# Performance work log

Measured on AMD Instinct MI355X. Metric: run time of the kernel, lower is better.

## Reference

```python
import jax, jax.numpy as jnp
import numpy as np

B, T, D = 2, 2048, 1024
NH, NKV, HD = 16, 4, 64
BASE, TSL, QGI = 10000.0, 1024, 1.5
EPS = 1.1920929e-07  # torch.finfo(float32).eps used by F.rms_norm default


def _rope_cos_sin(seq_len, rd):
    # Rotary.forward with self.rd == head_dim (Attn sets rd=0 -> full rotation)
    if seq_len > TSL:  # NTK-style base rescale branch
        nb = BASE * (seq_len / TSL) ** (rd / (rd - 2))
    else:
        nb = BASE
    inv = 1.0 / nb ** (jnp.arange(0, rd, 2, dtype=jnp.float32) / rd)
    fr = jnp.arange(seq_len, dtype=jnp.float32)[:, None] * inv[None, :]
    return jnp.cos(fr)[None, :, None, :], jnp.sin(fr)[None, :, None, :]


def _apply_rope(x, cos, sin):
    h = x.shape[-1] // 2
    x1, x2 = x[..., :h], x[..., h:]
    return jnp.concatenate([x1 * cos + x2 * sin, -x1 * sin + x2 * cos], axis=-1)


def _rms_norm(x):
    return x * jax.lax.rsqrt(jnp.mean(x * x, axis=-1, keepdims=True) + EPS)


def setup_inputs() -> dict:
    key = jax.random.key(0)
    ks = jax.random.split(key, 8)
    s = jnp.float32(0.02)
    return {
        "x": jax.random.normal(ks[0], (B, T, D), jnp.float32),
        "qw": jax.random.normal(ks[1], (NH * HD, D), jnp.float32) * s,
        "kw": jax.random.normal(ks[2], (NKV * HD, D), jnp.float32) * s,
        "vw": jax.random.normal(ks[3], (NKV * HD, D), jnp.float32) * s,
        "ow": jax.random.normal(ks[4], (D, D), jnp.float32) * s,
        "ve": jax.random.normal(ks[5], (B, T, NKV * HD), jnp.float32) * s,
        "v0": jax.random.normal(ks[6], (B, T, NKV, HD), jnp.float32) * s,
        "q_gain": jnp.full((NH,), QGI, jnp.float32),
        "vr_lambda": jnp.array([0.5, 0.5], jnp.float32),
        "gate_w": jnp.zeros((NH, D), jnp.float32),      # nn.init.zeros_
        "gate_b": jnp.full((NH,), 4.0, jnp.float32),    # nn.init.constant_(4.0)
    }


def reference(x, qw, kw, vw, ow, ve, v0, q_gain, vr_lambda, gate_w, gate_b):
    # projections
    q = (x @ qw.T).reshape(B, T, NH, HD)
    k = (x @ kw.T).reshape(B, T, NKV, HD)
    v = (x @ vw.T + ve).reshape(B, T, NKV, HD)
    raw_v = v  # returned when vr=True
    v = vr_lambda[0] * v0 + vr_lambda[1] * v  # value residual
    # qk rms-norm + rope (full head dim since self.rd == 0) + per-head q gain
    q = _rms_norm(q)
    k = _rms_norm(k)
    cos, sin = _rope_cos_sin(T, HD)
    q = _apply_rope(q, cos, sin)
    k = _apply_rope(k, cos, sin)
    q = q * q_gain[None, None, :, None]
    # causal GQA attention (nh query heads share nkv kv heads)
    G = NH // NKV
    qg = q.reshape(B, T, NKV, G, HD)
    scale = 1.0 / np.sqrt(HD).astype(np.float32)
    scores = jnp.einsum('bqhgd,bkhd->bhgqk', qg, k) * scale  # [B,NKV,G,T,T]
    causal = jnp.tril(jnp.ones((T, T), bool))
    scores = jnp.where(causal[None, None, None], scores, jnp.finfo(scores.dtype).min)
    p = jax.nn.softmax(scores, axis=-1)
    y = jnp.einsum('bhgqk,bkhd->bqhgd', p, v).reshape(B, T, NH, HD)
    # gated attention output
    gate = jax.nn.sigmoid(x @ gate_w.T + gate_b)  # [B,T,NH]
    y = y * gate[..., None]
    out = y.reshape(B, T, D) @ ow.T
    return out, raw_v
```

## Files before the change

### kernel.cpp

```cpp
#include <hip/hip_runtime.h>
#include <math.h>

#define BB 2
#define TT 2048
#define DD 1024
#define NH 16
#define NKV 4
#define HD 64
#define EPSF 1.1920929e-07f
#define LOG2_NB 14.319970444065578
#define SCALE_LOG2E 0.18033688011112042f
#define FIXMAX 17.5f

typedef __attribute__((ext_vector_type(8))) short bf16x8;
typedef __attribute__((ext_vector_type(4))) float f32x4;

__device__ inline short f2bf(float f) {
    unsigned u = __builtin_bit_cast(unsigned, f);
    unsigned r = (u + 0x7fffu + ((u >> 16) & 1u)) >> 16;
    return (short)r;
}
__device__ inline unsigned cvt_pk_bf16(float a, float b) {
    unsigned r;
    asm("v_cvt_pk_bf16_f32 %0, %1, %2" : "=v"(r) : "v"(a), "v"(b));
    return r;
}

__global__ __launch_bounds__(256) void conv_all(
    const float* __restrict__ x, const float* __restrict__ qw,
    const float* __restrict__ kw, const float* __restrict__ vw,
    const float* __restrict__ ow,
    short* __restrict__ x16, short* __restrict__ wb16, short* __restrict__ ow16)
{
    int i = blockIdx.x * 256 + threadIdx.x;
    const float* src; short* dst; int j;
    if (i < 1048576)      { src = x;  dst = x16;            j = i; }
    else if (i < 1310720) { src = qw; dst = wb16;           j = i - 1048576; }
    else if (i < 1376256) { src = kw; dst = wb16 + 1048576; j = i - 1310720; }
    else if (i < 1441792) { src = vw; dst = wb16 + 1310720; j = i - 1376256; }
    else                  { src = ow; dst = ow16;           j = i - 1441792; }
    float4 v = ((const float4*)src)[j];
    short4 o;
    o.x = f2bf(v.x); o.y = f2bf(v.y); o.z = f2bf(v.z); o.w = f2bf(v.w);
    ((short4*)dst)[j] = o;
}

__global__ __launch_bounds__(256, 4) void gemm_mfma(
    const short* __restrict__ A, const short* __restrict__ Bmat,
    float* __restrict__ C, int ldc, int klen)
{
    __shared__ short As[2][128*32];
    __shared__ short Bs[2][128*32];
    int tid = threadIdx.x;
    int w = tid >> 6, lane = tid & 63;
    int quad = lane >> 4, lc = lane & 15;
    int wy = w >> 1, wx = w & 1;
    int m0 = blockIdx.y * 128, n0 = blockIdx.x * 128;
    int kbeg = blockIdx.z * klen, kend = kbeg + klen;
    float* Cz = C + (size_t)blockIdx.z * 4096 * ldc;

    f32x4 acc[4][4];
    #pragma unroll
    for (int i = 0; i < 4; i++)
        #pragma unroll
        for (int j = 0; j < 4; j++) acc[i][j] = (f32x4){0.f,0.f,0.f,0.f};

    #define GSTAGE(buf, k0)                                                             \
    {                                                                                   \
        _Pragma("unroll")                                                               \
        for (int i = 0; i < 2; i++) {                                                   \
            int off = w*2048 + i*1024;                   \
            int g = (off >> 4) + lane;                               \
            int row = g >> 2, c = g & 3;                                                \
            int cg = c ^ (row & 3);                                    \
            const short* ga = A + (size_t)(m0 + row)*1024 + (k0) + cg*8;                \
            __builtin_amdgcn_global_load_lds(                                           \
                (const __attribute__((address_space(1))) void*)ga,                      \
                (__attribute__((address_space(3))) void*)((char*)&As[buf][0] + off), 16, 0, 0); \
            const short* gb = Bmat + (size_t)(n0 + row)*1024 + (k0) + cg*8;             \
            __builtin_amdgcn_global_load_lds(                                           \
                (const __attribute__((address_space(1))) void*)gb,                      \
                (__attribute__((address_space(3))) void*)((char*)&Bs[buf][0] + off), 16, 0, 0); \
        }                                                                               \
    }

    GSTAGE(0, kbeg);
    __syncthreads();

    for (int k0 = kbeg; k0 < kend; k0 += 32) {
        int cur = ((k0 - kbeg) >> 5) & 1;

        bf16x8 af[4], bfr[4];
        #pragma unroll
        for (int tm = 0; tm < 4; tm++) {
            int row = wy*64 + tm*16 + lc;
            af[tm] = *(const bf16x8*)(&As[cur][0] + row*32 + ((quad*8) ^ ((row&3)*8)));
        }
        #pragma unroll
        for (int tn = 0; tn < 4; tn++) {
            int row = wx*64 + tn*16 + lc;
            bfr[tn] = *(const bf16x8*)(&Bs[cur][0] + row*32 + ((quad*8) ^ ((row&3)*8)));
        }
        if (k0 + 32 < kend) GSTAGE(cur ^ 1, k0 + 32);
        #pragma unroll
        for (int tm = 0; tm < 4; tm++)
            #pragma unroll
            for (int tn = 0; tn < 4; tn++)
                acc[tm][tn] = __builtin_amdgcn_mfma_f32_16x16x32_bf16(af[tm], bfr[tn], acc[tm][tn], 0, 0, 0);
        __syncthreads();
    }

    #pragma unroll
    for (int tm = 0; tm < 4; tm++)
        #pragma unroll
        for (int r = 0; r < 4; r++) {
            int m = m0 + wy*64 + tm*16 + quad*4 + r;
            #pragma unroll
            for (int tn = 0; tn < 4; tn++) {
                int n = n0 + wx*64 + tn*16 + lc;
                Cz[(size_t)m*ldc + n] = acc[tm][tn][r];
            }
        }
}

__global__ __launch_bounds__(256) void qkv_epilogue(
    const float* __restrict__ qp0, const float* __restrict__ qp1,
    const float* __restrict__ ve, const float* __restrict__ v0,
    const float* __restrict__ q_gain, const float* __restrict__ vr_lambda,
    short* __restrict__ qbh, short* __restrict__ kbh, short* __restrict__ vb,
    float* __restrict__ rawv)
{
    int wave = blockIdx.x * 4 + (threadIdx.x >> 6);
    int lane = threadIdx.x & 63;
    int row = wave / 24;
    int hh  = wave % 24;
    int b = row >> 11;
    int t = row & (TT - 1);

    if (hh < 20) {
        int col = (hh < 16) ? (hh*64 + lane) : (1024 + (hh-16)*64 + lane);
        size_t idx = (size_t)row*1536 + col;
        float val = qp0[idx] + qp1[idx];
        float ss = val * val;
        #pragma unroll
        for (int off = 32; off; off >>= 1) ss += __shfl_xor(ss, off);
        val *= rsqrtf(ss * (1.0f/64.0f) + EPSF);
        float partner = __shfl(val, lane ^ 32);
        int idxr = lane & 31;
        float inv = (float)exp2((double)idxr * (-LOG2_NB / 32.0));
        float fr = (float)t * inv;
        float sn, cs;
        sincosf(fr, &sn, &cs);
        float outv = (lane < 32) ? (val*cs + partner*sn) : (val*cs - partner*sn);
        if (hh < 16) {
            outv *= q_gain[hh] * SCALE_LOG2E;
            qbh[(((size_t)(b*16 + hh))*2048 + t)*64 + lane] = f2bf(outv);
        } else {
            kbh[(((size_t)(b*4 + (hh-16)))*2048 + t)*64 + lane] = f2bf(outv);
        }
    } else {
        int vh = hh - 20;
        size_t off = ((size_t)row*4 + vh)*64 + lane;
        size_t idx = (size_t)row*1536 + 1280 + vh*64 + lane;
        float vraw = qp0[idx] + qp1[idx] + ve[off];
        rawv[off] = vraw;
        float vmix = vr_lambda[0]*v0[off] + vr_lambda[1]*vraw;
        vb[off] = f2bf(vmix);
    }
}

__global__ __launch_bounds__(256) void transpose_v(
    const short* __restrict__ vb, short* __restrict__ vtb)
{
    __shared__ short tile[64][72];
    int bk = blockIdx.x;
    int tt = blockIdx.y;
    int b = bk >> 2, kvh = bk & 3;
    int tid = threadIdx.x;
    int t4 = tid >> 4;
    int d4 = (tid & 15) * 4;
    #pragma unroll
    for (int i = 0; i < 4; i++) {
        int t = t4 + i*16;
        const short* src = vb + (((size_t)(b*2048 + tt*64 + t)*4 + kvh)*64 + d4);
        *(short4*)&tile[t][d4] = *(const short4*)src;
    }
    __syncthreads();
    #pragma unroll
    for (int i = 0; i < 4; i++) {
        int d = t4 + i*16;
        int t0 = d4;
        short4 o;
        o.x = tile[t0+0][d]; o.y = tile[t0+1][d];
        o.z = tile[t0+2][d]; o.w = tile[t0+3][d];
        *(short4*)&vtb[((size_t)(bk*64 + d))*2048 + tt*64 + t0] = o;
    }
}

__global__ __launch_bounds__(256) void gate_kernel(
    const float* __restrict__ x, const float* __restrict__ gw,
    const float* __restrict__ gb, float* __restrict__ gate)
{
    __shared__ float xs[1024];
    int row = blockIdx.x;
    int tid = threadIdx.x;
    *(float4*)&xs[tid*4] = *(const float4*)&x[(size_t)row*1024 + tid*4];
    __syncthreads();
    int wave = tid >> 6, lane = tid & 63;
    for (int h = wave; h < 16; h += 4) {
        const float* w = gw + (size_t)h * 1024;
        float s = 0.f;
        #pragma unroll
        for (int i = 0; i < 16; i++) s += xs[lane + 64*i] * w[lane + 64*i];
        #pragma unroll
        for (int off = 32; off; off >>= 1) s += __shfl_xor(s, off);
        if (lane == 0) gate[(size_t)row*16 + h] = 1.0f / (1.0f + __expf(-(s + gb[h])));
    }
}

__global__ __launch_bounds__(256, 4) void flash_mfma(
    const short* __restrict__ qbh, const short* __restrict__ kbh,
    const short* __restrict__ vtb, const float* __restrict__ gate,
    short* __restrict__ y16)
{
    __shared__ short Ks[2][64*64];
    __shared__ short Vt[2][64*64];
    __shared__ short Ps[4][16*64];

    int bh = blockIdx.x;
    int b = bh >> 4, h = bh & 15, kvh = h >> 2;
    int qt = 31 - blockIdx.y;
    int tid = threadIdx.x;
    int w = tid >> 6, lane = tid & 63;
    int quad = lane >> 4, lc = lane & 15;

    const short* qbase = qbh + (((size_t)bh)*2048 + qt*64 + w*16 + lc)*64;
    bf16x8 qf0 = *(const bf16x8*)(qbase + quad*8);
    bf16x8 qf1 = *(const bf16x8*)(qbase + 32 + quad*8);

    f32x4 o[4];
    #pragma unroll
    for (int i = 0; i < 4; i++) o[i] = (f32x4){0.f,0.f,0.f,0.f};
    f32x4 l4 = (f32x4){0.f,0.f,0.f,0.f};
    const bf16x8 ones = {(short)0x3F80,(short)0x3F80,(short)0x3F80,(short)0x3F80,
                         (short)0x3F80,(short)0x3F80,(short)0x3F80,(short)0x3F80};

    const size_t kbase = ((size_t)(b*4 + kvh))*2048*64;
    const size_t vbase = ((size_t)(b*4 + kvh))*64*2048;

    #define STAGE(buf, kt)                                                              \
    {                                                                                   \
        _Pragma("unroll")                                                               \
        for (int i = 0; i < 2; i++) {                                                   \
            int off = w*2048 + i*1024;                                                  \
            int g = (off >> 4) + lane;                                                  \
            int row = g >> 3, c = g & 7;                                                \
            int cg = c ^ (row & 7);                                                     \
            const short* gk = kbh + kbase + (size_t)((kt)*64 + row)*64 + cg*8;          \
            __builtin_amdgcn_global_load_lds(                                           \
                (const __attribute__((address_space(1))) void*)gk,                      \
                (__attribute__((address_space(3))) void*)((char*)Ks[buf] + off), 16, 0, 0); \
            const short* gv = vtb + vbase + (size_t)row*2048 + (kt)*64 + cg*8;          \
            __builtin_amdgcn_global_load_lds(                                           \
                (const __attribute__((address_space(1))) void*)gv,                      \
                (__attribute__((address_space(3))) void*)((char*)Vt[buf] + off), 16, 0, 0); \
        }                                                                               \
    }

    STAGE(0, 0);
    __syncthreads();

    short* ps = Ps[w];

    for (int kt = 0; kt <= qt; kt++) {
        int cur = kt & 1;
        bool diag = (kt == qt);

        bf16x8 kf0[4], kf1[4], vf0[4], vf1[4];
        #pragma unroll
        for (int kn = 0; kn < 4; kn++) {
            int row = kn*16 + lc;
            int sw = (row & 7) * 8;
            const short* kr = Ks[cur] + row*64;
            kf0[kn] = *(const bf16x8*)(kr + ((quad*8) ^ sw));
            kf1[kn] = *(const bf16x8*)(kr + ((quad*8 + 32) ^ sw));
            const short* vr = Vt[cur] + row*64;
            vf0[kn] = *(const bf16x8*)(vr + ((quad*8) ^ sw));
            vf1[kn] = *(const bf16x8*)(vr + ((quad*8 + 32) ^ sw));
        }
        if (kt < qt) STAGE(cur ^ 1, kt + 1);

        f32x4 s4[4];
        #pragma unroll
        for (int kn = 0; kn < 4; kn++) {
            f32x4 acc = (f32x4){0.f,0.f,0.f,0.f};
            acc = __builtin_amdgcn_mfma_f32_16x16x32_bf16(kf0[kn], qf0, acc, 0, 0, 0);
            acc = __builtin_amdgcn_mfma_f32_16x16x32_bf16(kf1[kn], qf1, acc, 0, 0, 0);
            s4[kn] = acc;
        }

        #pragma unroll
        for (int kn = 0; kn < 4; kn++) {
            float p0 = __builtin_amdgcn_exp2f(s4[kn][0] - FIXMAX);
            float p1 = __builtin_amdgcn_exp2f(s4[kn][1] - FIXMAX);
            float p2 = __builtin_amdgcn_exp2f(s4[kn][2] - FIXMAX);
            float p3 = __builtin_amdgcn_exp2f(s4[kn][3] - FIXMAX);
            if (diag) {
                int keyb = kn*16 + quad*4, qv = w*16 + lc;
                if (keyb + 0 > qv) p0 = 0.f;
                if (keyb + 1 > qv) p1 = 0.f;
                if (keyb + 2 > qv) p2 = 0.f;
                if (keyb + 3 > qv) p3 = 0.f;
            }
            int c = kn*4 + quad;
            int cs = c ^ ((lc & 7) << 1);
            int2 pk;
            pk.x = (int)cvt_pk_bf16(p0, p1);
            pk.y = (int)cvt_pk_bf16(p2, p3);
            *(int2*)(ps + lc*64 + cs*4) = pk;
        }
        __asm__ volatile("s_waitcnt lgkmcnt(0)" ::: "memory");
        int u0 = (0*4 + quad) ^ (lc & 7);
        int u1 = (1*4 + quad) ^ (lc & 7);
        bf16x8 pf0 = *(const bf16x8*)(ps + lc*64 + u0*8);
        bf16x8 pf1 = *(const bf16x8*)(ps + lc*64 + u1*8);

        #pragma unroll
        for (int dn = 0; dn < 4; dn++) {
            o[dn] = __builtin_amdgcn_mfma_f32_16x16x32_bf16(pf0, vf0[dn], o[dn], 0, 0, 0);
            o[dn] = __builtin_amdgcn_mfma_f32_16x16x32_bf16(pf1, vf1[dn], o[dn], 0, 0, 0);
        }
        l4 = __builtin_amdgcn_mfma_f32_16x16x32_bf16(pf0, ones, l4, 0, 0, 0);
        l4 = __builtin_amdgcn_mfma_f32_16x16x32_bf16(pf1, ones, l4, 0, 0, 0);
        __syncthreads();
    }

    #pragma unroll
    for (int r = 0; r < 4; r++) {
        int row = b*2048 + qt*64 + w*16 + quad*4 + r;
        float g = gate[(size_t)row*16 + h] / l4[r];
        #pragma unroll
        for (int dn = 0; dn < 4; dn++)
            y16[(size_t)row*1024 + h*64 + dn*16 + lc] = f2bf(o[dn][r] * g);
    }
}

extern "C" void kernel_launch(void* const* d_in, const int* in_sizes, int n_in,
                              void* d_out, int out_size, void* d_ws, size_t ws_size,
                              hipStream_t stream) {
    (void)in_sizes; (void)n_in; (void)out_size; (void)ws_size;
    const float* x  = (const float*)d_in[0];
    const float* qw = (const float*)d_in[1];
    const float* kw = (const float*)d_in[2];
    const float* vw = (const float*)d_in[3];
    const float* ow = (const float*)d_in[4];
    const float* ve = (const float*)d_in[5];
    const float* v0 = (const float*)d_in[6];
    const float* qg = (const float*)d_in[7];
    const float* vl = (const float*)d_in[8];
    const float* gw = (const float*)d_in[9];
    const float* gb = (const float*)d_in[10];

    float* out  = (float*)d_out;
    float* rawv = out + (size_t)BB*TT*DD;

    float* ws   = (float*)d_ws;
    float* qkvp = ws;
    float* p    = ws + 2*6291456;
    short* x16  = (short*)p;        p += 2097152;
    short* wb16 = (short*)p;        p += 786432;
    short* ow16 = (short*)p;        p += 524288;
    short* qbh  = (short*)p;        p += 2097152;
    short* kbh  = (short*)p;        p += 524288;
    short* vtb  = (short*)p;        p += 524288;
    short* vb   = (short*)p;        p += 524288;
    float* gt   = p;
    short* y16  = (short*)qkvp;

    conv_all<<<6656, 256, 0, stream>>>(x, qw, kw, vw, ow, x16, wb16, ow16);
    gemm_mfma<<<dim3(12, 32, 2), 256, 0, stream>>>(x16, wb16, qkvp, 1536, 512);
    qkv_epilogue<<<24576, 256, 0, stream>>>(qkvp, qkvp + 6291456, ve, v0, qg, vl,
                                            qbh, kbh, vb, rawv);
    transpose_v<<<dim3(8, 32), 256, 0, stream>>>(vb, vtb);
    gate_kernel<<<4096, 256, 0, stream>>>(x, gw, gb, gt);
    flash_mfma<<<dim3(32, 32), 256, 0, stream>>>(qbh, kbh, vtb, gt, y16);
    gemm_mfma<<<dim3(8, 32, 1), 256, 0, stream>>>(y16, ow16, out, 1024, 1024);
}
```

Baseline: 211.1 us.

## Fuse QKV epilogue into QKV GEMM and drop split-K partial buffers

The separate QKV epilogue kernel is replaced by an epilogue inside the QKV GEMM. It applies RMS-norm, RoPE, q gain and the value residual directly from the accumulators, using shuffles across the 16-lane column group. Split-K over two z-slices is removed, so the fp32 partial sums are no longer written and re-read, though the grid shrinks from 768 to 384 blocks and launch bounds drop to 3. The gate kernel now reads the bf16 copy of x instead of fp32, which loses some precision in the gate logits.

New measurement: 199.8 us. 1.06x faster.

```diff
diff --git a/kernel.cpp b/kernel.cpp
--- a/kernel.cpp
+++ b/kernel.cpp
@@ -19,6 +19,10 @@
     unsigned u = __builtin_bit_cast(unsigned, f);
     unsigned r = (u + 0x7fffu + ((u >> 16) & 1u)) >> 16;
     return (short)r;
+}
+__device__ inline float bf2f(short s) {
+    unsigned u = ((unsigned)(unsigned short)s) << 16;
+    return __builtin_bit_cast(float, u);
 }
 __device__ inline unsigned cvt_pk_bf16(float a, float b) {
     unsigned r;
@@ -45,9 +49,56 @@
     ((short4*)dst)[j] = o;
 }
 
-__global__ __launch_bounds__(256, 4) void gemm_mfma(
+#define GSTAGE(buf, k0, Abase, Bbase)                                                   \
+{                                                                                       \
+    _Pragma("unroll")                                                                   \
+    for (int i_ = 0; i_ < 2; i_++) {                                                    \
+        int off = w*2048 + i_*1024;                      \
+        int g = (off >> 4) + lane;                                   \
+        int row = g >> 2, c = g & 3;                                                    \
+        int cg = c ^ (row & 3);                                        \
+        const short* ga = (Abase) + (size_t)(m0 + row)*1024 + (k0) + cg*8;              \
+        __builtin_amdgcn_global_load_lds(                                               \
+            (const __attribute__((address_space(1))) void*)ga,                          \
+            (__attribute__((address_space(3))) void*)((char*)&As[buf][0] + off), 16, 0, 0); \
+        const short* gb = (Bbase) + (size_t)(n0 + row)*1024 + (k0) + cg*8;              \
+        __builtin_amdgcn_global_load_lds(                                               \
+            (const __attribute__((address_space(1))) void*)gb,                          \
+            (__attribute__((address_space(3))) void*)((char*)&Bs[buf][0] + off), 16, 0, 0); \
+    }                                                                                   \
+}
+
+#define GEMM_MAIN_LOOP(kbeg, kend, Abase, Bbase)                                        \
+    GSTAGE(0, (kbeg), (Abase), (Bbase));                                                \
+    __syncthreads();                                                                    \
+    for (int k0 = (kbeg); k0 < (kend); k0 += 32) {                                      \
+        int cur = ((k0 - (kbeg)) >> 5) & 1;                                             \
+        bf16x8 af[4], bfr[4];                                                           \
+        _Pragma("unroll")                                                               \
+        for (int tm = 0; tm < 4; tm++) {                                                \
+            int row = wy*64 + tm*16 + lc;                                               \
+            af[tm] = *(const bf16x8*)(&As[cur][0] + row*32 + ((quad*8) ^ ((row&3)*8))); \
+        }                                                                               \
+        _Pragma("unroll")                                                               \
+        for (int tn = 0; tn < 4; tn++) {                                                \
+            int row = wx*64 + tn*16 + lc;                                               \
+            bfr[tn] = *(const bf16x8*)(&Bs[cur][0] + row*32 + ((quad*8) ^ ((row&3)*8))); \
+        }                                                                               \
+        if (k0 + 32 < (kend)) GSTAGE(cur ^ 1, k0 + 32, (Abase), (Bbase));               \
+        _Pragma("unroll")                                                               \
+        for (int tm = 0; tm < 4; tm++)                                                  \
+            _Pragma("unroll")                                                           \
+            for (int tn = 0; tn < 4; tn++)                                              \
+                acc[tm][tn] = __builtin_amdgcn_mfma_f32_16x16x32_bf16(af[tm], bfr[tn], acc[tm][tn], 0, 0, 0); \
+        __syncthreads();                                                                \
+    }
+
+__global__ __launch_bounds__(256, 3) void gemm_qkv_fused(
     const short* __restrict__ A, const short* __restrict__ Bmat,
-    float* __restrict__ C, int ldc, int klen)
+    const float* __restrict__ ve, const float* __restrict__ v0,
+    const float* __restrict__ q_gain, const float* __restrict__ vr_lambda,
+    short* __restrict__ qbh, short* __restrict__ kbh, short* __restrict__ vb,
+    float* __restrict__ rawv)
 {
     __shared__ short As[2][128*32];
     __shared__ short Bs[2][128*32];
@@ -56,8 +107,6 @@
     int quad = lane >> 4, lc = lane & 15;
     int wy = w >> 1, wx = w & 1;
     int m0 = blockIdx.y * 128, n0 = blockIdx.x * 128;
-    int kbeg = blockIdx.z * klen, kend = kbeg + klen;
-    float* Cz = C + (size_t)blockIdx.z * 4096 * ldc;
 
     f32x4 acc[4][4];
     #pragma unroll
@@ -65,50 +114,85 @@
         #pragma unroll
         for (int j = 0; j < 4; j++) acc[i][j] = (f32x4){0.f,0.f,0.f,0.f};
 
-    #define GSTAGE(buf, k0)                                                             \
-    {                                                                                   \
-        _Pragma("unroll")                                                               \
-        for (int i = 0; i < 2; i++) {                                                   \
-            int off = w*2048 + i*1024;                   \
-            int g = (off >> 4) + lane;                               \
-            int row = g >> 2, c = g & 3;                                                \
-            int cg = c ^ (row & 3);                                    \
-            const short* ga = A + (size_t)(m0 + row)*1024 + (k0) + cg*8;                \
-            __builtin_amdgcn_global_load_lds(                                           \
-                (const __attribute__((address_space(1))) void*)ga,                      \
-                (__attribute__((address_space(3))) void*)((char*)&As[buf][0] + off), 16, 0, 0); \
-            const short* gb = Bmat + (size_t)(n0 + row)*1024 + (k0) + cg*8;             \
-            __builtin_amdgcn_global_load_lds(                                           \
-                (const __attribute__((address_space(1))) void*)gb,                      \
-                (__attribute__((address_space(3))) void*)((char*)&Bs[buf][0] + off), 16, 0, 0); \
-        }                                                                               \
-    }
-
-    GSTAGE(0, kbeg);
-    __syncthreads();
-
-    for (int k0 = kbeg; k0 < kend; k0 += 32) {
-        int cur = ((k0 - kbeg) >> 5) & 1;
-
-        bf16x8 af[4], bfr[4];
+    GEMM_MAIN_LOOP(0, 1024, A, Bmat);
+
+    int hc = n0 + wx*64;
+    if (hc < 1280) {
+        bool isq = (hc < 1024);
+        int h = isq ? (hc >> 6) : ((hc - 1024) >> 6);
+        float gsc = isq ? (q_gain[h] * SCALE_LOG2E) : 1.0f;
+        short* dst = isq ? qbh : kbh;
+        int nhh = isq ? 16 : 4;
+        float inv0 = (float)exp2((double)lc * (-LOG2_NB / 32.0));
+        float inv1 = (float)exp2((double)(lc + 16) * (-LOG2_NB / 32.0));
         #pragma unroll
         for (int tm = 0; tm < 4; tm++) {
-            int row = wy*64 + tm*16 + lc;
-            af[tm] = *(const bf16x8*)(&As[cur][0] + row*32 + ((quad*8) ^ ((row&3)*8)));
-        }
-        #pragma unroll
-        for (int tn = 0; tn < 4; tn++) {
-            int row = wx*64 + tn*16 + lc;
-            bfr[tn] = *(const bf16x8*)(&Bs[cur][0] + row*32 + ((quad*8) ^ ((row&3)*8)));
-        }
-        if (k0 + 32 < kend) GSTAGE(cur ^ 1, k0 + 32);
-        #pragma unroll
-        for (int tm = 0; tm < 4; tm++)
             #pragma unroll
-            for (int tn = 0; tn < 4; tn++)
-                acc[tm][tn] = __builtin_amdgcn_mfma_f32_16x16x32_bf16(af[tm], bfr[tn], acc[tm][tn], 0, 0, 0);
-        __syncthreads();
-    }
+            for (int r = 0; r < 4; r++) {
+                int m = m0 + wy*64 + tm*16 + quad*4 + r;
+                int b = m >> 11, t = m & (TT - 1);
+                float a0 = acc[tm][0][r], a1 = acc[tm][1][r];
+                float a2 = acc[tm][2][r], a3 = acc[tm][3][r];
+                float ss = a0*a0 + a1*a1 + a2*a2 + a3*a3;
+                ss += __shfl_xor(ss, 1);
+                ss += __shfl_xor(ss, 2);
+                ss += __shfl_xor(ss, 4);
+                ss += __shfl_xor(ss, 8);
+                float rn = rsqrtf(ss * (1.0f/64.0f) + EPSF);
+                a0 *= rn; a1 *= rn; a2 *= rn; a3 *= rn;
+                float sn0, cs0, sn1, cs1;
+                sincosf((float)t * inv0, &sn0, &cs0);
+                sincosf((float)t * inv1, &sn1, &cs1);
+                float o0 = a0*cs0 + a2*sn0;
+                float o1 = a1*cs1 + a3*sn1;
+                float o2 = a2*cs0 - a0*sn0;
+                float o3 = a3*cs1 - a1*sn1;
+                size_t base = (((size_t)(b*nhh + h))*2048 + t)*64 + lc;
+                dst[base +  0] = f2bf(o0 * gsc);
+                dst[base + 16] = f2bf(o1 * gsc);
+                dst[base + 32] = f2bf(o2 * gsc);
+                dst[base + 48] = f2bf(o3 * gsc);
+            }
+        }
+    } else {
+        int vh = (hc - 1280) >> 6;
+        float l0 = vr_lambda[0], l1 = vr_lambda[1];
+        #pragma unroll
+        for (int tm = 0; tm < 4; tm++) {
+            #pragma unroll
+            for (int r = 0; r < 4; r++) {
+                int m = m0 + wy*64 + tm*16 + quad*4 + r;
+                size_t off = (size_t)m*256 + vh*64 + lc;
+                #pragma unroll
+                for (int tn = 0; tn < 4; tn++) {
+                    float val = acc[tm][tn][r] + ve[off + tn*16];
+                    rawv[off + tn*16] = val;
+                    vb[off + tn*16] = f2bf(l0 * v0[off + tn*16] + l1 * val);
+                }
+            }
+        }
+    }
+}
+
+__global__ __launch_bounds__(256, 4) void gemm_mfma(
+    const short* __restrict__ A, const short* __restrict__ Bmat,
+    float* __restrict__ C, int ldc, int klen)
+{
+    __shared__ short As[2][128*32];
+    __shared__ short Bs[2][128*32];
+    int tid = threadIdx.x;
+    int w = tid >> 6, lane = tid & 63;
+    int quad = lane >> 4, lc = lane & 15;
+    int wy = w >> 1, wx = w & 1;
+    int m0 = blockIdx.y * 128, n0 = blockIdx.x * 128;
+
+    f32x4 acc[4][4];
+    #pragma unroll
+    for (int i = 0; i < 4; i++)
+        #pragma unroll
+        for (int j = 0; j < 4; j++) acc[i][j] = (f32x4){0.f,0.f,0.f,0.f};
+
+    GEMM_MAIN_LOOP(0, klen, A, Bmat);
 
     #pragma unroll
     for (int tm = 0; tm < 4; tm++)
@@ -118,55 +202,9 @@
             #pragma unroll
             for (int tn = 0; tn < 4; tn++) {
                 int n = n0 + wx*64 + tn*16 + lc;
-                Cz[(size_t)m*ldc + n] = acc[tm][tn][r];
+                C[(size_t)m*ldc + n] = acc[tm][tn][r];
             }
         }
-}
-
-__global__ __launch_bounds__(256) void qkv_epilogue(
-    const float* __restrict__ qp0, const float* __restrict__ qp1,
-    const float* __restrict__ ve, const float* __restrict__ v0,
-    const float* __restrict__ q_gain, const float* __restrict__ vr_lambda,
-    short* __restrict__ qbh, short* __restrict__ kbh, short* __restrict__ vb,
-    float* __restrict__ rawv)
-{
-    int wave = blockIdx.x * 4 + (threadIdx.x >> 6);
-    int lane = threadIdx.x & 63;
-    int row = wave / 24;
-    int hh  = wave % 24;
-    int b = row >> 11;
-    int t = row & (TT - 1);
-
-    if (hh < 20) {
-        int col = (hh < 16) ? (hh*64 + lane) : (1024 + (hh-16)*64 + lane);
-        size_t idx = (size_t)row*1536 + col;
-        float val = qp0[idx] + qp1[idx];
-        float ss = val * val;
-        #pragma unroll
-        for (int off = 32; off; off >>= 1) ss += __shfl_xor(ss, off);
-        val *= rsqrtf(ss * (1.0f/64.0f) + EPSF);
-        float partner = __shfl(val, lane ^ 32);
-        int idxr = lane & 31;
-        float inv = (float)exp2((double)idxr * (-LOG2_NB / 32.0));
-        float fr = (float)t * inv;
-        float sn, cs;
-        sincosf(fr, &sn, &cs);
-        float outv = (lane < 32) ? (val*cs + partner*sn) : (val*cs - partner*sn);
-        if (hh < 16) {
-            outv *= q_gain[hh] * SCALE_LOG2E;
-            qbh[(((size_t)(b*16 + hh))*2048 + t)*64 + lane] = f2bf(outv);
-        } else {
-            kbh[(((size_t)(b*4 + (hh-16)))*2048 + t)*64 + lane] = f2bf(outv);
-        }
-    } else {
-        int vh = hh - 20;
-        size_t off = ((size_t)row*4 + vh)*64 + lane;
-        size_t idx = (size_t)row*1536 + 1280 + vh*64 + lane;
-        float vraw = qp0[idx] + qp1[idx] + ve[off];
-        rawv[off] = vraw;
-        float vmix = vr_lambda[0]*v0[off] + vr_lambda[1]*vraw;
-        vb[off] = f2bf(vmix);
-    }
 }
 
 __global__ __launch_bounds__(256) void transpose_v(
@@ -198,13 +236,15 @@
 }
 
 __global__ __launch_bounds__(256) void gate_kernel(
-    const float* __restrict__ x, const float* __restrict__ gw,
+    const short* __restrict__ x16, const float* __restrict__ gw,
     const float* __restrict__ gb, float* __restrict__ gate)
 {
     __shared__ float xs[1024];
     int row = blockIdx.x;
     int tid = threadIdx.x;
-    *(float4*)&xs[tid*4] = *(const float4*)&x[(size_t)row*1024 + tid*4];
+    short4 sv = *(const short4*)&x16[(size_t)row*1024 + tid*4];
+    xs[tid*4+0] = bf2f(sv.x); xs[tid*4+1] = bf2f(sv.y);
+    xs[tid*4+2] = bf2f(sv.z); xs[tid*4+3] = bf2f(sv.w);
     __syncthreads();
     int wave = tid >> 6, lane = tid & 63;
     for (int h = wave; h < 16; h += 4) {
@@ -364,9 +404,7 @@
     float* out  = (float*)d_out;
     float* rawv = out + (size_t)BB*TT*DD;
 
-    float* ws   = (float*)d_ws;
-    float* qkvp = ws;
-    float* p    = ws + 2*6291456;
+    float* p    = (float*)d_ws;
     short* x16  = (short*)p;        p += 2097152;
     short* wb16 = (short*)p;        p += 786432;
     short* ow16 = (short*)p;        p += 524288;
@@ -374,15 +412,14 @@
     short* kbh  = (short*)p;        p += 524288;
     short* vtb  = (short*)p;        p += 524288;
     short* vb   = (short*)p;        p += 524288;
-    float* gt   = p;
-    short* y16  = (short*)qkvp;
+    float* gt   = p;                p += 65536;
+    short* y16  = (short*)p;
 
     conv_all<<<6656, 256, 0, stream>>>(x, qw, kw, vw, ow, x16, wb16, ow16);
-    gemm_mfma<<<dim3(12, 32, 2), 256, 0, stream>>>(x16, wb16, qkvp, 1536, 512);
-    qkv_epilogue<<<24576, 256, 0, stream>>>(qkvp, qkvp + 6291456, ve, v0, qg, vl,
-                                            qbh, kbh, vb, rawv);
+    gemm_qkv_fused<<<dim3(12, 32), 256, 0, stream>>>(x16, wb16, ve, v0, qg, vl,
+                                                     qbh, kbh, vb, rawv);
     transpose_v<<<dim3(8, 32), 256, 0, stream>>>(vb, vtb);
-    gate_kernel<<<4096, 256, 0, stream>>>(x, gw, gb, gt);
+    gate_kernel<<<4096, 256, 0, stream>>>(x16, gw, gb, gt);
     flash_mfma<<<dim3(32, 32), 256, 0, stream>>>(qbh, kbh, vtb, gt, y16);
-    gemm_mfma<<<dim3(8, 32, 1), 256, 0, stream>>>(y16, ow16, out, 1024, 1024);
-}
+    gemm_mfma<<<dim3(8, 32), 256, 0, stream>>>(y16, ow16, out, 1024, 1024);
+}
```
